# Kernel optimization log

Measured on AMD Instinct MI355X. Metric: run time of the kernel, lower is better.

Reference implementation:

```python
import jax, jax.numpy as jnp
import numpy as np

N_NODES = 2048
N_GRAPHS = 64
N_EDGES = 16384
B = 65536
META = 64
TX = 8
NOISE = 128
IN_DIM = N_NODES + 1 + 32 + TX  # 2089


def setup_inputs() -> dict:
    key = jax.random.key(0)
    ks = jax.random.split(key, 11)
    return {
        "batched_graphs": jax.random.randint(ks[0], (B,), 0, N_GRAPHS),
        "batched_chain": jax.random.normal(ks[1], (B,), dtype=jnp.float32),
        "trigger_data": jax.random.normal(ks[2], (B, META), dtype=jnp.float32),
        "tx_start_time": jax.random.normal(ks[3], (B, TX), dtype=jnp.float32),
        "edges": jax.random.randint(ks[4], (N_GRAPHS, 2, N_EDGES), 0, N_NODES),
        "gcn_w": jax.random.normal(ks[5], (), dtype=jnp.float32),
        "gcn_b": jax.random.normal(ks[6], (), dtype=jnp.float32) * 0.01,
        "trig_W": jax.random.normal(ks[7], (META, 32), dtype=jnp.float32) / np.sqrt(META),
        "trig_b": jnp.zeros((32,), dtype=jnp.float32),
        "emb_W": jax.random.normal(ks[8], (IN_DIM, NOISE), dtype=jnp.float32) / np.sqrt(IN_DIM),
        "emb_b": jnp.zeros((NOISE,), dtype=jnp.float32),
    }


def _gcn_one_graph(edge_index, w, b):
    # GCNConv(1,1) on x = ones(n_nodes,1): add self loops, sym-normalize.
    self_idx = jnp.arange(N_NODES, dtype=edge_index.dtype)
    src = jnp.concatenate([edge_index[0], self_idx])
    dst = jnp.concatenate([edge_index[1], self_idx])
    deg = jax.ops.segment_sum(jnp.ones(src.shape[0], jnp.float32), dst,
                              num_segments=N_NODES)
    dinv = jnp.where(deg > 0, jax.lax.rsqrt(deg), 0.0)
    norm = dinv[src] * dinv[dst]
    agg = jax.ops.segment_sum(norm, dst, num_segments=N_NODES)  # [n_nodes]
    return agg * w + b  # x @ W with x==1 is just w per node, plus bias


def reference(batched_graphs, batched_chain, trigger_data, tx_start_time,
              edges, gcn_w, gcn_b, trig_W, trig_b, emb_W, emb_b):
    # Per-graph GCN embeddings for all topologies (covers all uniques). [G, n_nodes]
    graph_emb = jax.vmap(lambda e: _gcn_one_graph(e, gcn_w, gcn_b))(edges)
    ge = graph_emb[batched_graphs]                         # [B, n_nodes] gather
    trig = jax.nn.relu(trigger_data @ trig_W + trig_b)     # [B, 32]
    x = jnp.concatenate(
        [ge, batched_chain[:, None], trig, tx_start_time], axis=1)  # [B, IN_DIM]
    return x @ emb_W + emb_b                               # [B, NOISE]
```

## Files before the change

### kernel.cpp

```cpp
#include <hip/hip_runtime.h>

#define NN 2048
#define NG 64
#define NE 16384
#define BB 65536
#define META 64
#define TXD 8
#define NOISE 128


__global__ __launch_bounds__(512) void agg_kernel(
    const int* __restrict__ edges,
    const float* __restrict__ gcn_w,
    const float* __restrict__ gcn_b,
    float* __restrict__ emb,
    float* __restrict__ graph_out)
{
    __shared__ int   s_cnt[NN];
    __shared__ float s_dinv[NN];
    __shared__ float s_val[NN];
    const int g = blockIdx.x, tid = threadIdx.x;
    const int4* __restrict__ e4 = (const int4*)(edges + (size_t)g * 2 * NE);

    if (tid < NOISE) graph_out[g * NOISE + tid] = 0.0f;

    int4 ds[8];
    #pragma unroll
    for (int k = 0; k < 8; ++k) ds[k] = e4[4096 + k * 512 + tid];

    for (int n = tid; n < NN; n += 512) { s_cnt[n] = 1; s_val[n] = 0.0f; }
    __syncthreads();

    #pragma unroll
    for (int k = 0; k < 8; ++k) {
        atomicAdd(&s_cnt[ds[k].x], 1);
        atomicAdd(&s_cnt[ds[k].y], 1);
        atomicAdd(&s_cnt[ds[k].z], 1);
        atomicAdd(&s_cnt[ds[k].w], 1);
    }
    __syncthreads();
    for (int n = tid; n < NN; n += 512) s_dinv[n] = rsqrtf((float)s_cnt[n]);
    __syncthreads();

    #pragma unroll
    for (int k = 0; k < 8; ++k) {
        int4 sr = e4[k * 512 + tid];
        unsafeAtomicAdd(&s_val[ds[k].x], s_dinv[sr.x]);
        unsafeAtomicAdd(&s_val[ds[k].y], s_dinv[sr.y]);
        unsafeAtomicAdd(&s_val[ds[k].z], s_dinv[sr.z]);
        unsafeAtomicAdd(&s_val[ds[k].w], s_dinv[sr.w]);
    }
    __syncthreads();

    const float w = gcn_w[0], b = gcn_b[0];
    for (int n = tid; n < NN; n += 512) {
        float di = s_dinv[n];
        emb[(size_t)g * NN + n] = di * (s_val[n] + di) * w + b;
    }
}

__global__ __launch_bounds__(256) void fold_kernel(
    const float* __restrict__ emb,
    const float* __restrict__ emb_W,
    float* __restrict__ graph_out)
{
    __shared__ float s_e[128];
    __shared__ float s_red[128];
    const int tid = threadIdx.x;
    const int g = blockIdx.x >> 4, chunk = blockIdx.x & 15;
    const int n0 = chunk * 128;
    if (tid < 128) s_e[tid] = emb[(size_t)g * NN + n0 + tid];
    __syncthreads();
    const int c = tid & 127, h = tid >> 7;
    const float* __restrict__ Wp = emb_W + (size_t)(n0 + h * 64) * NOISE + c;
    const float* __restrict__ ep = s_e + h * 64;
    float a0 = 0.f, a1 = 0.f, a2 = 0.f, a3 = 0.f;
    #pragma unroll
    for (int i = 0; i < 64; i += 4) {
        a0 = fmaf(ep[i + 0], Wp[(i + 0) * NOISE], a0);
        a1 = fmaf(ep[i + 1], Wp[(i + 1) * NOISE], a1);
        a2 = fmaf(ep[i + 2], Wp[(i + 2) * NOISE], a2);
        a3 = fmaf(ep[i + 3], Wp[(i + 3) * NOISE], a3);
    }
    float acc = (a0 + a1) + (a2 + a3);
    if (h == 1) s_red[c] = acc;
    __syncthreads();
    if (h == 0) unsafeAtomicAdd(&graph_out[g * NOISE + c], acc + s_red[c]);
}

#define ROWS 32
__global__ __launch_bounds__(256, 3) void main_kernel(
    const int* __restrict__ bg,
    const float* __restrict__ chain,
    const float* __restrict__ trig_in,
    const float* __restrict__ txs,
    const float* __restrict__ trig_W,
    const float* __restrict__ trig_b,
    const float* __restrict__ emb_W,
    const float* __restrict__ emb_b,
    const float* __restrict__ graph_out,
    float* __restrict__ out)
{
    __shared__ float s_td[ROWS * 68];
    __shared__ float s_twT[32 * 68];
    __shared__ float s_trig[ROWS * 36];
    __shared__ float s_tx[ROWS * TXD];
    __shared__ float s_ch[ROWS];
    __shared__ int   s_gi[ROWS];

    const int tid = threadIdx.x;
    const int row0 = blockIdx.x * ROWS;

    {
        const float4* __restrict__ gsrc =
            (const float4*)(trig_in + (size_t)row0 * META);
        #pragma unroll
        for (int k = 0; k < 2; ++k) {
            int t = tid + k * 256;
            int r = t >> 4, i4 = t & 15;
            *(float4*)&s_td[r * 68 + i4 * 4] = gsrc[t];
        }
    }
    {
        const float4* __restrict__ gsrc = (const float4*)trig_W;
        #pragma unroll
        for (int k = 0; k < 2; ++k) {
            int t = tid + k * 256;
            int i = t >> 3, j4 = (t & 7) * 4;
            float4 v = gsrc[t];
            s_twT[(j4 + 0) * 68 + i] = v.x;
            s_twT[(j4 + 1) * 68 + i] = v.y;
            s_twT[(j4 + 2) * 68 + i] = v.z;
            s_twT[(j4 + 3) * 68 + i] = v.w;
        }
    }
    if (tid < 64) {
        int r = tid >> 1, k4 = (tid & 1) * 4;
        *(float4*)&s_tx[r * TXD + k4] =
            ((const float4*)(txs + (size_t)row0 * TXD))[tid];
    } else if (tid < 96) {
        int r = tid - 64;
        s_ch[r] = chain[row0 + r];
    } else if (tid < 128) {
        int r = tid - 96;
        s_gi[r] = bg[row0 + r];
    }

    const int n0 = (tid & 63) * 2;
    float2 w2[32], w3[TXD];
    #pragma unroll
    for (int j = 0; j < 32; ++j)
        w2[j] = *(const float2*)&emb_W[(size_t)(2049 + j) * NOISE + n0];
    #pragma unroll
    for (int k = 0; k < TXD; ++k)
        w3[k] = *(const float2*)&emb_W[(size_t)(2081 + k) * NOISE + n0];
    const float2 w1   = *(const float2*)&emb_W[(size_t)2048 * NOISE + n0];
    const float2 bias = *(const float2*)&emb_b[n0];

    __syncthreads();

    {
        const int j0 = tid & 15;
        const int r0 = (tid >> 4) * 2;
        const float* __restrict__ tw0 = s_twT + j0 * 68;
        const float* __restrict__ tw1 = s_twT + (j0 + 16) * 68;
        const float* __restrict__ td0 = s_td + r0 * 68;
        const float* __restrict__ td1 = s_td + (r0 + 1) * 68;
        float b0 = trig_b[j0], b1 = trig_b[j0 + 16];
        float a00 = b0, a01 = b1, a10 = b0, a11 = b1;
        #pragma unroll
        for (int i = 0; i < META; i += 4) {
            float4 u0 = *(const float4*)(tw0 + i);
            float4 u1 = *(const float4*)(tw1 + i);
            float4 t0 = *(const float4*)(td0 + i);
            float4 t1 = *(const float4*)(td1 + i);
            a00 = fmaf(t0.x, u0.x, a00); a00 = fmaf(t0.y, u0.y, a00);
            a00 = fmaf(t0.z, u0.z, a00); a00 = fmaf(t0.w, u0.w, a00);
            a01 = fmaf(t0.x, u1.x, a01); a01 = fmaf(t0.y, u1.y, a01);
            a01 = fmaf(t0.z, u1.z, a01); a01 = fmaf(t0.w, u1.w, a01);
            a10 = fmaf(t1.x, u0.x, a10); a10 = fmaf(t1.y, u0.y, a10);
            a10 = fmaf(t1.z, u0.z, a10); a10 = fmaf(t1.w, u0.w, a10);
            a11 = fmaf(t1.x, u1.x, a11); a11 = fmaf(t1.y, u1.y, a11);
            a11 = fmaf(t1.z, u1.z, a11); a11 = fmaf(t1.w, u1.w, a11);
        }
        s_trig[r0 * 36 + j0]            = fmaxf(a00, 0.f);
        s_trig[r0 * 36 + j0 + 16]       = fmaxf(a01, 0.f);
        s_trig[(r0 + 1) * 36 + j0]      = fmaxf(a10, 0.f);
        s_trig[(r0 + 1) * 36 + j0 + 16] = fmaxf(a11, 0.f);
    }
    __syncthreads();

    const int wv = tid >> 6;
    int   gs[8];
    float chs[8];
    #pragma unroll
    for (int p = 0; p < 8; ++p) {
        const int r = p * 4 + wv;
        gs[p]  = s_gi[r];
        chs[p] = s_ch[r];
    }
    float2 go[8];
    #pragma unroll
    for (int p = 0; p < 8; ++p)
        go[p] = *(const float2*)&graph_out[gs[p] * NOISE + n0];

    #pragma unroll
    for (int p = 0; p < 8; ++p) {
        const int r = p * 4 + wv;
        const int row = row0 + r;
        float ax = bias.x + go[p].x + chs[p] * w1.x;
        float ay = bias.y + go[p].y + chs[p] * w1.y;
        const float4* __restrict__ tx4 = (const float4*)(s_tx + r * TXD);
        float4 t0 = tx4[0], t1 = tx4[1];
        ax = fmaf(t0.x, w3[0].x, ax); ay = fmaf(t0.x, w3[0].y, ay);
        ax = fmaf(t0.y, w3[1].x, ax); ay = fmaf(t0.y, w3[1].y, ay);
        ax = fmaf(t0.z, w3[2].x, ax); ay = fmaf(t0.z, w3[2].y, ay);
        ax = fmaf(t0.w, w3[3].x, ax); ay = fmaf(t0.w, w3[3].y, ay);
        ax = fmaf(t1.x, w3[4].x, ax); ay = fmaf(t1.x, w3[4].y, ay);
        ax = fmaf(t1.y, w3[5].x, ax); ay = fmaf(t1.y, w3[5].y, ay);
        ax = fmaf(t1.z, w3[6].x, ax); ay = fmaf(t1.z, w3[6].y, ay);
        ax = fmaf(t1.w, w3[7].x, ax); ay = fmaf(t1.w, w3[7].y, ay);
        const float* __restrict__ tg = s_trig + r * 36;
        #pragma unroll
        for (int q = 0; q < 8; ++q) {
            float4 t4 = *(const float4*)(tg + q * 4);
            ax = fmaf(t4.x, w2[4 * q + 0].x, ax); ay = fmaf(t4.x, w2[4 * q + 0].y, ay);
            ax = fmaf(t4.y, w2[4 * q + 1].x, ax); ay = fmaf(t4.y, w2[4 * q + 1].y, ay);
            ax = fmaf(t4.z, w2[4 * q + 2].x, ax); ay = fmaf(t4.z, w2[4 * q + 2].y, ay);
            ax = fmaf(t4.w, w2[4 * q + 3].x, ax); ay = fmaf(t4.w, w2[4 * q + 3].y, ay);
        }
        *(float2*)&out[(size_t)row * NOISE + n0] = make_float2(ax, ay);
    }
}

extern "C" void kernel_launch(void* const* d_in, const int* in_sizes, int n_in,
                              void* d_out, int out_size, void* d_ws, size_t ws_size,
                              hipStream_t stream) {
    const int*   bg      = (const int*)d_in[0];
    const float* chain   = (const float*)d_in[1];
    const float* trig_in = (const float*)d_in[2];
    const float* txs     = (const float*)d_in[3];
    const int*   edges   = (const int*)d_in[4];
    const float* gcn_w   = (const float*)d_in[5];
    const float* gcn_b   = (const float*)d_in[6];
    const float* trig_W  = (const float*)d_in[7];
    const float* trig_b  = (const float*)d_in[8];
    const float* emb_W   = (const float*)d_in[9];
    const float* emb_b   = (const float*)d_in[10];
    float* out = (float*)d_out;

    float* graph_out = (float*)d_ws;
    float* emb       = (float*)d_ws + NG * NOISE;

    agg_kernel<<<NG, 512, 0, stream>>>(edges, gcn_w, gcn_b, emb, graph_out);
    fold_kernel<<<NG * 16, 256, 0, stream>>>(emb, emb_W, graph_out);
    main_kernel<<<BB / ROWS, 256, 0, stream>>>(bg, chain, trig_in, txs, trig_W,
                                               trig_b, emb_W, emb_b, graph_out, out);
}
```

Measured before the change: 145.0 us.

## Fuse GCN aggregation and emb_W fold into a single per-graph kernel

```diff
diff --git a/kernel.cpp b/kernel.cpp
--- a/kernel.cpp
+++ b/kernel.cpp
@@ -9,20 +9,19 @@
 #define NOISE 128
 
 
-__global__ __launch_bounds__(512) void agg_kernel(
+__global__ __launch_bounds__(512) void gcn_kernel(
     const int* __restrict__ edges,
     const float* __restrict__ gcn_w,
     const float* __restrict__ gcn_b,
-    float* __restrict__ emb,
+    const float* __restrict__ emb_W,
     float* __restrict__ graph_out)
 {
     __shared__ int   s_cnt[NN];
     __shared__ float s_dinv[NN];
     __shared__ float s_val[NN];
+    __shared__ float s_part[4][NOISE];
     const int g = blockIdx.x, tid = threadIdx.x;
     const int4* __restrict__ e4 = (const int4*)(edges + (size_t)g * 2 * NE);
-
-    if (tid < NOISE) graph_out[g * NOISE + tid] = 0.0f;
 
     int4 ds[8];
     #pragma unroll
@@ -55,37 +54,31 @@
     const float w = gcn_w[0], b = gcn_b[0];
     for (int n = tid; n < NN; n += 512) {
         float di = s_dinv[n];
-        emb[(size_t)g * NN + n] = di * (s_val[n] + di) * w + b;
-    }
-}
-
-__global__ __launch_bounds__(256) void fold_kernel(
-    const float* __restrict__ emb,
-    const float* __restrict__ emb_W,
-    float* __restrict__ graph_out)
-{
-    __shared__ float s_e[128];
-    __shared__ float s_red[128];
-    const int tid = threadIdx.x;
-    const int g = blockIdx.x >> 4, chunk = blockIdx.x & 15;
-    const int n0 = chunk * 128;
-    if (tid < 128) s_e[tid] = emb[(size_t)g * NN + n0 + tid];
-    __syncthreads();
-    const int c = tid & 127, h = tid >> 7;
-    const float* __restrict__ Wp = emb_W + (size_t)(n0 + h * 64) * NOISE + c;
-    const float* __restrict__ ep = s_e + h * 64;
+        s_val[n] = di * (s_val[n] + di) * w + b;
+    }
+    __syncthreads();
+
+    const int c = tid & 127, q = tid >> 7;
+    const float* __restrict__ Wp = emb_W + (size_t)(q * 512) * NOISE + c;
+    const float* __restrict__ ep = s_val + q * 512;
     float a0 = 0.f, a1 = 0.f, a2 = 0.f, a3 = 0.f;
-    #pragma unroll
-    for (int i = 0; i < 64; i += 4) {
+    float a4 = 0.f, a5 = 0.f, a6 = 0.f, a7 = 0.f;
+    #pragma unroll 2
+    for (int i = 0; i < 512; i += 8) {
         a0 = fmaf(ep[i + 0], Wp[(i + 0) * NOISE], a0);
         a1 = fmaf(ep[i + 1], Wp[(i + 1) * NOISE], a1);
         a2 = fmaf(ep[i + 2], Wp[(i + 2) * NOISE], a2);
         a3 = fmaf(ep[i + 3], Wp[(i + 3) * NOISE], a3);
-    }
-    float acc = (a0 + a1) + (a2 + a3);
-    if (h == 1) s_red[c] = acc;
-    __syncthreads();
-    if (h == 0) unsafeAtomicAdd(&graph_out[g * NOISE + c], acc + s_red[c]);
+        a4 = fmaf(ep[i + 4], Wp[(i + 4) * NOISE], a4);
+        a5 = fmaf(ep[i + 5], Wp[(i + 5) * NOISE], a5);
+        a6 = fmaf(ep[i + 6], Wp[(i + 6) * NOISE], a6);
+        a7 = fmaf(ep[i + 7], Wp[(i + 7) * NOISE], a7);
+    }
+    s_part[q][c] = ((a0 + a1) + (a2 + a3)) + ((a4 + a5) + (a6 + a7));
+    __syncthreads();
+    if (tid < NOISE)
+        graph_out[g * NOISE + tid] = (s_part[0][tid] + s_part[1][tid])
+                                   + (s_part[2][tid] + s_part[3][tid]);
 }
 
 #define ROWS 32
@@ -250,10 +243,8 @@
     float* out = (float*)d_out;
 
     float* graph_out = (float*)d_ws;
-    float* emb       = (float*)d_ws + NG * NOISE;
-
-    agg_kernel<<<NG, 512, 0, stream>>>(edges, gcn_w, gcn_b, emb, graph_out);
-    fold_kernel<<<NG * 16, 256, 0, stream>>>(emb, emb_W, graph_out);
+
+    gcn_kernel<<<NG, 512, 0, stream>>>(edges, gcn_w, gcn_b, emb_W, graph_out);
     main_kernel<<<BB / ROWS, 256, 0, stream>>>(bg, chain, trig_in, txs, trig_W,
                                                trig_b, emb_W, emb_b, graph_out, out);
 }
```

New measurement: 152.0 us. +4.8%, slower.
